# Performance work log

Measured on AMD Instinct MI355X. Metric: run time of the kernel, lower is better.

The kernel has to match this reference:

```python
import jax, jax.numpy as jnp
import numpy as np

INF = 1.0e9
B, NI, NJ = 1, 768, 768
C_NODE, C_PAIR = 512, 128
H, C_HID = 8, 32
LN_EPS = 1e-5


def _ln(x, w, b):
    m = jnp.mean(x, axis=-1, keepdims=True)
    v = jnp.mean(jnp.square(x - m), axis=-1, keepdims=True)
    return (x - m) * jax.lax.rsqrt(v + LN_EPS) * w + b


def setup_inputs() -> dict:
    key = jax.random.key(0)
    ks = jax.random.split(key, 16)
    s_node = 1.0 / np.sqrt(C_NODE)
    s_pair = 1.0 / np.sqrt(C_PAIR)
    s_hid = 1.0 / np.sqrt(H * C_HID)
    inp = {
        "node_embed_i": jax.random.normal(ks[0], (B, NI, C_NODE), jnp.float32),
        "node_embed_j": jax.random.normal(ks[1], (B, NJ, C_NODE), jnp.float32),
        "pair_embed": jax.random.normal(ks[2], (B, NI, NJ, C_PAIR), jnp.float32),
        "pair_mask": (jax.random.uniform(ks[3], (B, NI, NJ)) < 0.95).astype(jnp.float32),
        "node_mask_i": (jax.random.uniform(ks[4], (B, NI)) < 0.98).astype(jnp.float32),
        # LayerNorm params
        "ln_i_w": jnp.ones((C_NODE,), jnp.float32), "ln_i_b": jnp.zeros((C_NODE,), jnp.float32),
        "ln_j_w": jnp.ones((C_NODE,), jnp.float32), "ln_j_b": jnp.zeros((C_NODE,), jnp.float32),
        "ln_p_w": jnp.ones((C_PAIR,), jnp.float32), "ln_p_b": jnp.zeros((C_PAIR,), jnp.float32),
        # pair-bias projection and its gate: Linear(C_PAIR, H)
        "W_pb": jax.random.normal(ks[5], (C_PAIR, H), jnp.float32) * s_pair,
        "b_pb": jnp.zeros((H,), jnp.float32),
        "W_pg": jax.random.normal(ks[6], (C_PAIR, H), jnp.float32) * s_pair,
        "b_pg": jnp.zeros((H,), jnp.float32),
        # attention projections (q/k/v bias-free, OpenFold-style)
        "Wq": jax.random.normal(ks[7], (C_NODE, H * C_HID), jnp.float32) * s_node,
        "Wk": jax.random.normal(ks[8], (C_NODE, H * C_HID), jnp.float32) * s_node,
        "Wv": jax.random.normal(ks[9], (C_NODE, H * C_HID), jnp.float32) * s_node,
        # output gate and output projection
        "Wg": jax.random.normal(ks[10], (C_NODE, H * C_HID), jnp.float32) * s_node,
        "bg": jnp.zeros((H * C_HID,), jnp.float32),
        "Wo": jax.random.normal(ks[11], (H * C_HID, C_NODE), jnp.float32) * s_hid,
        "bo": jnp.zeros((C_NODE,), jnp.float32),
    }
    return inp


def reference(node_embed_i, node_embed_j, pair_embed, pair_mask, node_mask_i,
              ln_i_w, ln_i_b, ln_j_w, ln_j_b, ln_p_w, ln_p_b,
              W_pb, b_pb, W_pg, b_pg, Wq, Wk, Wv, Wg, bg, Wo, bo):
    # LayerNorms
    qx = _ln(node_embed_i, ln_i_w, ln_i_b)           # [B,NI,C_NODE]
    kx = _ln(node_embed_j, ln_j_w, ln_j_b)           # [B,NJ,C_NODE]
    p = _ln(pair_embed, ln_p_w, ln_p_b)              # [B,NI,NJ,C_PAIR]

    # additive mask bias: 0 where valid, -inf where masked; broadcast over heads
    mask_bias = (INF * (pair_mask - 1.0))[:, None, :, :]          # [B,1,NI,NJ]

    # gated pair bias -> [B,H,NI,NJ] (permute_final_dims([2,0,1]))
    pb = (p @ W_pb + b_pb) * jax.nn.sigmoid(p @ W_pg + b_pg)      # [B,NI,NJ,H]
    pair_bias = jnp.transpose(pb, (0, 3, 1, 2))

    # multi-head attention with injected biases
    q = (qx @ Wq).reshape(B, NI, H, C_HID) * (C_HID ** -0.5)
    k = (kx @ Wk).reshape(B, NJ, H, C_HID)
    v = (kx @ Wv).reshape(B, NJ, H, C_HID)
    scores = jnp.einsum('bihc,bjhc->bhij', q, k) + mask_bias + pair_bias
    a = jax.nn.softmax(scores, axis=-1)                           # [B,H,NI,NJ]
    o = jnp.einsum('bhij,bjhc->bihc', a, v)                       # [B,NI,H,C_HID]

    # sigmoid output gate, flatten heads, output projection
    g = jax.nn.sigmoid(qx @ Wg + bg).reshape(B, NI, H, C_HID)
    o = (o * g).reshape(B, NI, H * C_HID)
    mha_out = o @ Wo + bo                                         # [B,NI,C_NODE]

    # residual on the layernormed input, scaled by node mask (dropout = identity at inference)
    return qx + mha_out * node_mask_i[..., None]
```

## Files before the change

### kernel.cpp

```cpp
#include <hip/hip_runtime.h>
#include <hip/hip_bf16.h>

#define NI 768
#define NJ 768
#define CN 512
#define CP 128
#define NH 8
#define CH 32
#define HC 256
#define NSTR 6
#define SJ 128

typedef float  fx4  __attribute__((ext_vector_type(4)));
typedef float  fx2  __attribute__((ext_vector_type(2)));
typedef short  bv8  __attribute__((ext_vector_type(8)));
typedef unsigned short usx4 __attribute__((ext_vector_type(4)));

__device__ __forceinline__ short f2bf(float f) {
    __hip_bfloat16 h = __float2bfloat16(f);
    return *reinterpret_cast<short*>(&h);
}
__device__ __forceinline__ float bf2f(unsigned short u) {
    union { unsigned int u; float f; } c; c.u = ((unsigned int)u) << 16; return c.f;
}

__global__ __launch_bounds__(256) void fused_front_kernel(
    const float* __restrict__ node_i, const float* __restrict__ node_j,
    const float* __restrict__ ln_i_w, const float* __restrict__ ln_i_b,
    const float* __restrict__ ln_j_w, const float* __restrict__ ln_j_b,
    const float* __restrict__ Wq, const float* __restrict__ Wk,
    const float* __restrict__ Wv, const float* __restrict__ Wg,
    const float* __restrict__ bg,
    const float* __restrict__ lnpw, const float* __restrict__ lnpb,
    const float* __restrict__ Wpb, const float* __restrict__ bpb,
    const float* __restrict__ Wpg, const float* __restrict__ bpg,
    const float* __restrict__ pair, const float* __restrict__ pmask,
    float* __restrict__ qx, unsigned short* __restrict__ qsb,
    unsigned short* __restrict__ ksb, unsigned short* __restrict__ vtb,
    float* __restrict__ gs, unsigned short* __restrict__ biasb)
{
    const int bid = blockIdx.x;
    const int t = threadIdx.x;
    if (bid < 192) {
        __shared__ float xs[8][CN];
        __shared__ float red[4][8][2];
        const bool isj = bid >= 96;
        const int r0 = (isj ? bid - 96 : bid) * 8;
        const float* xin = isj ? node_j : node_i;
        const float* lw = isj ? ln_j_w : ln_i_w;
        const float* lb = isj ? ln_j_b : ln_i_b;
        const int wv = t >> 6;

        fx2 vrow[8]; float s8[8], q8[8];
#pragma unroll
        for (int r = 0; r < 8; ++r) {
            vrow[r] = *(const fx2*)(xin + (size_t)(r0 + r) * CN + t * 2);
            s8[r] = vrow[r][0] + vrow[r][1];
            q8[r] = vrow[r][0] * vrow[r][0] + vrow[r][1] * vrow[r][1];
        }
#pragma unroll
        for (int d = 1; d < 64; d <<= 1)
#pragma unroll
            for (int r = 0; r < 8; ++r) {
                s8[r] += __shfl_xor(s8[r], d);
                q8[r] += __shfl_xor(q8[r], d);
            }
        if ((t & 63) == 0)
#pragma unroll
            for (int r = 0; r < 8; ++r) { red[wv][r][0] = s8[r]; red[wv][r][1] = q8[r]; }
        __syncthreads();
        fx2 lwv = *(const fx2*)(lw + t * 2), lbv = *(const fx2*)(lb + t * 2);
#pragma unroll
        for (int r = 0; r < 8; ++r) {
            float s = red[0][r][0] + red[1][r][0] + red[2][r][0] + red[3][r][0];
            float q = red[0][r][1] + red[1][r][1] + red[2][r][1] + red[3][r][1];
            float mean = s * (1.f / CN);
            float var = q * (1.f / CN) - mean * mean;
            float rs = rsqrtf(var + 1e-5f);
            fx2 o;
            o[0] = (vrow[r][0] - mean) * rs * lwv[0] + lbv[0];
            o[1] = (vrow[r][1] - mean) * rs * lwv[1] + lbv[1];
            xs[r][t * 2] = o[0]; xs[r][t * 2 + 1] = o[1];
            if (!isj) *(fx2*)(qx + (size_t)(r0 + r) * CN + t * 2) = o;
        }
        __syncthreads();

        for (int m = 0; m < 2; ++m) {
            const float* W = isj ? (m ? Wv : Wk) : (m ? Wg : Wq);
            float acc[8] = {0.f,0.f,0.f,0.f,0.f,0.f,0.f,0.f};
            for (int cc = 0; cc < CN; cc += 4) {
                fx4 xv[8];
#pragma unroll
                for (int r = 0; r < 8; ++r) xv[r] = *(const fx4*)&xs[r][cc];
#pragma unroll
                for (int u = 0; u < 4; ++u) {
                    float w = W[(size_t)(cc + u) * HC + t];
#pragma unroll
                    for (int r = 0; r < 8; ++r) acc[r] = fmaf(xv[r][u], w, acc[r]);
                }
            }
            if (!isj) {
                if (m == 0) {
#pragma unroll
                    for (int r = 0; r < 8; ++r)
                        qsb[(size_t)(r0 + r) * HC + t] =
                            (unsigned short)f2bf(acc[r] * 0.17677669529663687f);
                } else {
#pragma unroll
                    for (int r = 0; r < 8; ++r)
                        gs[(size_t)(r0 + r) * HC + t] =
                            1.f / (1.f + __expf(-(acc[r] + bg[t])));
                }
            } else {
                if (m == 0) {
#pragma unroll
                    for (int r = 0; r < 8; ++r)
                        ksb[(size_t)(r0 + r) * HC + t] = (unsigned short)f2bf(acc[r]);
                } else {
                    bv8 vv;
#pragma unroll
                    for (int r = 0; r < 8; ++r) vv[r] = f2bf(acc[r]);
                    *(bv8*)&vtb[(size_t)t * NJ + r0] = vv;
                }
            }
        }
        return;
    }

    __shared__ unsigned short wcatT[16][136];
    __shared__ float redS[16][16], redC[16][16];
    __shared__ float scalS[16], scalC[16];
    __shared__ unsigned short sb[8][68];

    const int lane = t & 63;
    const int wave = t >> 6;
    const int bid2 = bid - 192;
    const int i    = bid2 / 12;
    const int jt64 = (bid2 % 12) * 64;
    const int jt   = jt64 + wave * 16;
    const int o  = lane & 15;
    const int kq = lane >> 4;

    for (int rep = 0; rep < 2; ++rep) {
        const float* prow = pair + ((size_t)i * NJ + (jt + o)) * CP + kq * 8;
        fx4 x0[4], x1[4];
#pragma unroll
        for (int s = 0; s < 4; ++s) {
            x0[s] = *(const fx4*)(prow + s * 32);
            x1[s] = *(const fx4*)(prow + s * 32 + 4);
        }

        {
            const int oo = t & 15, cg = t >> 4;
            float pS = 0.f, pC = 0.f;
#pragma unroll
            for (int e = 0; e < 8; ++e) {
                int c = cg * 8 + e;
                float w = (oo < 8) ? Wpb[c * 8 + oo] : Wpg[c * 8 + (oo - 8)];
                float wv = lnpw[c] * w;
                short b = f2bf(wv);
                wcatT[oo][c] = (unsigned short)b;
                pS += bf2f((unsigned short)b);
                pC += lnpb[c] * w;
            }
            redS[cg][oo] = pS; redC[cg][oo] = pC;
            __syncthreads();
            if (t < 16) {
                float s = 0.f, c2 = 0.f;
#pragma unroll
                for (int k = 0; k < 16; ++k) { s += redS[k][t]; c2 += redC[k][t]; }
                scalS[t] = s;
                scalC[t] = c2 + ((t < 8) ? bpb[t] : bpg[t - 8]);
            }
            __syncthreads();
        }

        bv8 bfrag[4];
#pragma unroll
        for (int s = 0; s < 4; ++s)
            bfrag[s] = *(const bv8*)&wcatT[o][s * 32 + kq * 8];
        const float spb = scalS[o];
        const float cpb = scalC[o];

        bv8 afrag[4];
#pragma unroll
        for (int s = 0; s < 4; ++s) {
#pragma unroll
            for (int u = 0; u < 4; ++u) {
                afrag[s][u]     = f2bf(x0[s][u]);
                afrag[s][u + 4] = f2bf(x1[s][u]);
            }
        }
        bv8 ones;
#pragma unroll
        for (int u = 0; u < 8; ++u) ones[u] = (short)0x3F80;

        fx4 acc  = {0.f, 0.f, 0.f, 0.f};
        fx4 accS = {0.f, 0.f, 0.f, 0.f};
        fx4 accG = {0.f, 0.f, 0.f, 0.f};
#pragma unroll
        for (int s = 0; s < 4; ++s) {
            acc  = __builtin_amdgcn_mfma_f32_16x16x32_bf16(afrag[s], bfrag[s], acc,  0, 0, 0);
            accS = __builtin_amdgcn_mfma_f32_16x16x32_bf16(afrag[s], ones,     accS, 0, 0, 0);
            accG = __builtin_amdgcn_mfma_f32_16x16x32_bf16(afrag[s], afrag[s], accG, 0, 0, 0);
        }

#pragma unroll
        for (int r = 0; r < 4; ++r) {
            const int p = kq * 4 + r;
            float sp = accS[r];
            float qp = __shfl(accG[r], kq * 20 + r);
            float mean = sp * (1.f / CP);
            float var  = qp * (1.f / CP) - mean * mean;
            float rstd = rsqrtf(var + 1e-5f);
            float pre  = rstd * (acc[r] - mean * spb) + cpb;
            float part = __shfl_xor(pre, 8);
            if (o < 8) {
                float sig = 1.f / (1.f + __expf(-part));
                int j = jt + p;
                float b = pre * sig + (pmask[(size_t)i * NJ + j] - 1.f) * 1.0e9f;
                sb[o][wave * 16 + p] = (unsigned short)f2bf(b);
            }
        }
        __syncthreads();
        if (t < 128) {
            const int oo = t >> 4, ck = t & 15;
            usx4 v;
#pragma unroll
            for (int u = 0; u < 4; ++u) v[u] = sb[oo][ck * 4 + u];
            *(usx4*)&biasb[((size_t)oo * NI + i) * NJ + jt64 + ck * 4] = v;
        }
        __syncthreads();
    }
}

__global__ __launch_bounds__(256) void attn_kernel(
    const short* __restrict__ qsb, const short* __restrict__ ksb,
    const short* __restrict__ vtb, const unsigned short* __restrict__ biasb,
    float* __restrict__ pnum, float* __restrict__ pden)
{
    __shared__ unsigned short P[32][136];
    __shared__ float sumbuf[4][32];
    const int i0 = blockIdx.x * 32;
    const int h  = blockIdx.y;
    const int jbase = blockIdx.z * SJ;
    const int pb = ((int)blockIdx.x * NH + h) * NSTR + blockIdx.z;
    const int t = threadIdx.x;
    const int w = t >> 6;
    const int lane = t & 63;
    const int rowl = lane & 15;
    const int g = lane >> 4;

    bv8 aq[2];
#pragma unroll
    for (int it = 0; it < 2; ++it)
        aq[it] = *(const bv8*)&qsb[(size_t)(i0 + it * 16 + rowl) * HC + h * CH + g * 8];

    bv8 bk[2];
#pragma unroll
    for (int jt = 0; jt < 2; ++jt) {
        const int jb = jbase + w * 32 + jt * 16;
        bk[jt] = *(const bv8*)&ksb[(size_t)(jb + rowl) * HC + h * CH + g * 8];
    }
    const unsigned short* bbase = biasb + (size_t)h * NI * NJ;
    unsigned short bl[2][2][4];
#pragma unroll
    for (int jt = 0; jt < 2; ++jt) {
        const int jb = jbase + w * 32 + jt * 16;
#pragma unroll
        for (int it = 0; it < 2; ++it)
#pragma unroll
            for (int r = 0; r < 4; ++r) {
                const int il = it * 16 + g * 4 + r;
                bl[jt][it][r] = bbase[(size_t)(i0 + il) * NJ + jb + rowl];
            }
    }

    float rs[2][4] = {{0.f,0.f,0.f,0.f},{0.f,0.f,0.f,0.f}};
#pragma unroll
    for (int jt = 0; jt < 2; ++jt) {
        const int jloc = w * 32 + jt * 16;
#pragma unroll
        for (int it = 0; it < 2; ++it) {
            fx4 acc = {0.f, 0.f, 0.f, 0.f};
            acc = __builtin_amdgcn_mfma_f32_16x16x32_bf16(aq[it], bk[jt], acc, 0, 0, 0);
#pragma unroll
            for (int r = 0; r < 4; ++r) {
                const int il = it * 16 + g * 4 + r;
                float s = acc[r] + bf2f(bl[jt][it][r]);
                float p = __expf(s);
                rs[it][r] += p;
                P[il][jloc + rowl] = (unsigned short)f2bf(p);
            }
        }
    }
#pragma unroll
    for (int it = 0; it < 2; ++it)
#pragma unroll
        for (int r = 0; r < 4; ++r) {
            float v = rs[it][r];
            v += __shfl_xor(v, 1); v += __shfl_xor(v, 2);
            v += __shfl_xor(v, 4); v += __shfl_xor(v, 8);
            rs[it][r] = v;
        }
    if (rowl == 0) {
#pragma unroll
        for (int it = 0; it < 2; ++it)
#pragma unroll
            for (int r = 0; r < 4; ++r)
                sumbuf[w][it * 16 + g * 4 + r] = rs[it][r];
    }

    const int it = w & 1, ct = w >> 1;
    bv8 vv[4];
#pragma unroll
    for (int kk = 0; kk < 4; ++kk)
        vv[kk] = *(const bv8*)&vtb[(size_t)(h * CH + ct * 16 + rowl) * NJ + jbase + kk * 32 + g * 8];

    __syncthreads();

    if (t < 32)
        pden[(size_t)pb * 32 + t] =
            sumbuf[0][t] + sumbuf[1][t] + sumbuf[2][t] + sumbuf[3][t];

    fx4 acc = {0.f, 0.f, 0.f, 0.f};
#pragma unroll
    for (int kk = 0; kk < 4; ++kk) {
        bv8 ap = *(const bv8*)&P[it * 16 + rowl][kk * 32 + g * 8];
        acc = __builtin_amdgcn_mfma_f32_16x16x32_bf16(ap, vv[kk], acc, 0, 0, 0);
    }
#pragma unroll
    for (int r = 0; r < 4; ++r) {
        const int il = it * 16 + g * 4 + r;
        pnum[(size_t)pb * 1024 + il * 32 + ct * 16 + rowl] = acc[r];
    }
}

__global__ __launch_bounds__(256) void combine_out_kernel(
    const float* __restrict__ pnum, const float* __restrict__ pden,
    const float* __restrict__ gs, const float* __restrict__ qx,
    const float* __restrict__ Wo, const float* __restrict__ bo,
    const float* __restrict__ mi, float* __restrict__ outp)
{
    __shared__ float ogl[2][HC];
    const int r0 = blockIdx.x * 2;
    const int t = threadIdx.x;
    const int h = t >> 5, c = t & 31;
#pragma unroll
    for (int r = 0; r < 2; ++r) {
        const int i = r0 + r;
        const int pb = ((i >> 5) * NH + h) * NSTR;
        const int il = i & 31;
        float n = 0.f, d = 0.f;
#pragma unroll
        for (int s = 0; s < NSTR; ++s) {
            n += pnum[(size_t)(pb + s) * 1024 + il * 32 + c];
            d += pden[(size_t)(pb + s) * 32 + il];
        }
        ogl[r][t] = n / d * gs[(size_t)i * HC + t];
    }
    __syncthreads();

    float acc[2][2] = {{0,0},{0,0}};
    for (int cc = 0; cc < HC; cc += 4) {
        fx4 xr0 = *(const fx4*)&ogl[0][cc];
        fx4 xr1 = *(const fx4*)&ogl[1][cc];
#pragma unroll
        for (int u = 0; u < 4; ++u) {
            float w0 = Wo[(size_t)(cc + u) * CN + t];
            float w1 = Wo[(size_t)(cc + u) * CN + 256 + t];
            acc[0][0] = fmaf(xr0[u], w0, acc[0][0]); acc[0][1] = fmaf(xr0[u], w1, acc[0][1]);
            acc[1][0] = fmaf(xr1[u], w0, acc[1][0]); acc[1][1] = fmaf(xr1[u], w1, acc[1][1]);
        }
    }
#pragma unroll
    for (int r = 0; r < 2; ++r) {
        float mk = mi[r0 + r];
        size_t base = (size_t)(r0 + r) * CN;
        outp[base + t]       = qx[base + t]       + (acc[r][0] + bo[t])       * mk;
        outp[base + 256 + t] = qx[base + 256 + t] + (acc[r][1] + bo[t + 256]) * mk;
    }
}

extern "C" void kernel_launch(void* const* d_in, const int* in_sizes, int n_in,
                              void* d_out, int out_size, void* d_ws, size_t ws_size,
                              hipStream_t stream)
{
    const float* node_i = (const float*)d_in[0];
    const float* node_j = (const float*)d_in[1];
    const float* pair   = (const float*)d_in[2];
    const float* pmask  = (const float*)d_in[3];
    const float* nmask  = (const float*)d_in[4];
    const float* ln_i_w = (const float*)d_in[5];
    const float* ln_i_b = (const float*)d_in[6];
    const float* ln_j_w = (const float*)d_in[7];
    const float* ln_j_b = (const float*)d_in[8];
    const float* ln_p_w = (const float*)d_in[9];
    const float* ln_p_b = (const float*)d_in[10];
    const float* W_pb   = (const float*)d_in[11];
    const float* b_pb   = (const float*)d_in[12];
    const float* W_pg   = (const float*)d_in[13];
    const float* b_pg   = (const float*)d_in[14];
    const float* Wq     = (const float*)d_in[15];
    const float* Wk     = (const float*)d_in[16];
    const float* Wv     = (const float*)d_in[17];
    const float* Wg     = (const float*)d_in[18];
    const float* bg     = (const float*)d_in[19];
    const float* Wo     = (const float*)d_in[20];
    const float* bo     = (const float*)d_in[21];
    float* outp = (float*)d_out;

    float* fw = (float*)d_ws;
    float* qx   = fw;
    float* gs   = qx + (size_t)NI * CN;
    float* pnum = gs + (size_t)NI * HC;
    float* pden = pnum + (size_t)24 * NH * NSTR * 1024;
    unsigned short* qsb = (unsigned short*)(pden + (size_t)24 * NH * NSTR * 32);
    unsigned short* ksb = qsb + (size_t)NI * HC;
    unsigned short* vtb = ksb + (size_t)NJ * HC;
    unsigned short* biasb = vtb + (size_t)HC * NJ;

    hipLaunchKernelGGL(fused_front_kernel, dim3(192 + (NI * NJ) / 64), dim3(256), 0, stream,
                       node_i, node_j, ln_i_w, ln_i_b, ln_j_w, ln_j_b,
                       Wq, Wk, Wv, Wg, bg,
                       ln_p_w, ln_p_b, W_pb, b_pb, W_pg, b_pg,
                       pair, pmask,
                       qx, qsb, ksb, vtb, gs, biasb);
    hipLaunchKernelGGL(attn_kernel, dim3(NI / 32, NH, NSTR), dim3(256), 0, stream,
                       (const short*)qsb, (const short*)ksb, (const short*)vtb,
                       biasb, pnum, pden);
    hipLaunchKernelGGL(combine_out_kernel, dim3(NI / 2), dim3(256), 0, stream,
                       pnum, pden, gs, qx, Wo, bo, nmask, outp);
}
```

Measured before the change: 124.3 us.

## Fuse all three stages into one persistent cooperative kernel with grid syncs

Adds a persistent mega-kernel that runs the node LayerNorm and projections, the pair-bias computation, the attention strips and the output combine. Each stage uses grid-stride loops and the stages are separated by cooperative grid barriers, launched with an occupancy-sized grid. It also drops the redundant two-iteration repeat of the pair-bias block, which recomputed and re-read the large pair tensor. The goal is to remove inter-kernel launch gaps and duplicated pair traffic. The trade-offs are grid-wide barrier costs and less latency hiding from the persistent scheduling. The old three-kernel path stays as a fallback.

```diff
diff --git a/kernel.cpp b/kernel.cpp
--- a/kernel.cpp
+++ b/kernel.cpp
@@ -1,5 +1,8 @@
 #include <hip/hip_runtime.h>
 #include <hip/hip_bf16.h>
+#include <hip/hip_cooperative_groups.h>
+
+namespace cg = cooperative_groups;
 
 #define NI 768
 #define NJ 768
@@ -22,6 +25,362 @@
 }
 __device__ __forceinline__ float bf2f(unsigned short u) {
     union { unsigned int u; float f; } c; c.u = ((unsigned int)u) << 16; return c.f;
+}
+
+struct NodeS { float xs[8][CN]; float red[4][8][2]; };
+struct PairS { float redS[16][16]; float redC[16][16]; unsigned short sb[8][68]; };
+struct AttnS { unsigned short P[32][136]; float sumbuf[4][32]; };
+struct CombS { float ogl[2][HC]; };
+union SmemU { NodeS n; PairS p; AttnS a; CombS c; };
+
+__global__ __launch_bounds__(256) void mega_kernel(
+    const float* __restrict__ node_i, const float* __restrict__ node_j,
+    const float* __restrict__ ln_i_w, const float* __restrict__ ln_i_b,
+    const float* __restrict__ ln_j_w, const float* __restrict__ ln_j_b,
+    const float* __restrict__ Wq, const float* __restrict__ Wk,
+    const float* __restrict__ Wv, const float* __restrict__ Wg,
+    const float* __restrict__ bg,
+    const float* __restrict__ lnpw, const float* __restrict__ lnpb,
+    const float* __restrict__ Wpb, const float* __restrict__ bpb,
+    const float* __restrict__ Wpg, const float* __restrict__ bpg,
+    const float* __restrict__ pair, const float* __restrict__ pmask,
+    const float* __restrict__ mi,
+    const float* __restrict__ Wo, const float* __restrict__ bo,
+    float* __restrict__ qx, unsigned short* __restrict__ qsb,
+    unsigned short* __restrict__ ksb, unsigned short* __restrict__ vtb,
+    float* __restrict__ gs, unsigned short* __restrict__ biasb,
+    float* __restrict__ pnum, float* __restrict__ pden,
+    float* __restrict__ outp)
+{
+    __shared__ SmemU sm;
+    __shared__ unsigned short wcatT[16][136];
+    __shared__ float scalS[16], scalC[16];
+
+    cg::grid_group gg = cg::this_grid();
+    const int bid = blockIdx.x;
+    const int gsz = gridDim.x;
+    const int t = threadIdx.x;
+    const int lane = t & 63, wave = t >> 6;
+    const int o = lane & 15, kq = lane >> 4;
+
+    {
+        const int oo = t & 15, cgi = t >> 4;
+        float pS = 0.f, pC = 0.f;
+#pragma unroll
+        for (int e = 0; e < 8; ++e) {
+            int c = cgi * 8 + e;
+            float w = (oo < 8) ? Wpb[c * 8 + oo] : Wpg[c * 8 + (oo - 8)];
+            float wv = lnpw[c] * w;
+            short b = f2bf(wv);
+            wcatT[oo][c] = (unsigned short)b;
+            pS += bf2f((unsigned short)b);
+            pC += lnpb[c] * w;
+        }
+        sm.p.redS[cgi][oo] = pS; sm.p.redC[cgi][oo] = pC;
+        __syncthreads();
+        if (t < 16) {
+            float s = 0.f, c2 = 0.f;
+#pragma unroll
+            for (int k = 0; k < 16; ++k) { s += sm.p.redS[k][t]; c2 += sm.p.redC[k][t]; }
+            scalS[t] = s;
+            scalC[t] = c2 + ((t < 8) ? bpb[t] : bpg[t - 8]);
+        }
+        __syncthreads();
+    }
+
+    for (int unit = bid; unit < 192 + (NI * NJ) / 64; unit += gsz) {
+        if (unit < 192) {
+            const bool isj = unit >= 96;
+            const int r0 = (isj ? unit - 96 : unit) * 8;
+            const float* xin = isj ? node_j : node_i;
+            const float* lw = isj ? ln_j_w : ln_i_w;
+            const float* lb = isj ? ln_j_b : ln_i_b;
+
+            fx2 vrow[8]; float s8[8], q8[8];
+#pragma unroll
+            for (int r = 0; r < 8; ++r) {
+                vrow[r] = *(const fx2*)(xin + (size_t)(r0 + r) * CN + t * 2);
+                s8[r] = vrow[r][0] + vrow[r][1];
+                q8[r] = vrow[r][0] * vrow[r][0] + vrow[r][1] * vrow[r][1];
+            }
+#pragma unroll
+            for (int d = 1; d < 64; d <<= 1)
+#pragma unroll
+                for (int r = 0; r < 8; ++r) {
+                    s8[r] += __shfl_xor(s8[r], d);
+                    q8[r] += __shfl_xor(q8[r], d);
+                }
+            if ((t & 63) == 0)
+#pragma unroll
+                for (int r = 0; r < 8; ++r) { sm.n.red[wave][r][0] = s8[r]; sm.n.red[wave][r][1] = q8[r]; }
+            __syncthreads();
+            fx2 lwv = *(const fx2*)(lw + t * 2), lbv = *(const fx2*)(lb + t * 2);
+#pragma unroll
+            for (int r = 0; r < 8; ++r) {
+                float s = sm.n.red[0][r][0] + sm.n.red[1][r][0] + sm.n.red[2][r][0] + sm.n.red[3][r][0];
+                float q = sm.n.red[0][r][1] + sm.n.red[1][r][1] + sm.n.red[2][r][1] + sm.n.red[3][r][1];
+                float mean = s * (1.f / CN);
+                float var = q * (1.f / CN) - mean * mean;
+                float rs = rsqrtf(var + 1e-5f);
+                fx2 ov;
+                ov[0] = (vrow[r][0] - mean) * rs * lwv[0] + lbv[0];
+                ov[1] = (vrow[r][1] - mean) * rs * lwv[1] + lbv[1];
+                sm.n.xs[r][t * 2] = ov[0]; sm.n.xs[r][t * 2 + 1] = ov[1];
+                if (!isj) *(fx2*)(qx + (size_t)(r0 + r) * CN + t * 2) = ov;
+            }
+            __syncthreads();
+
+            for (int m = 0; m < 2; ++m) {
+                const float* W = isj ? (m ? Wv : Wk) : (m ? Wg : Wq);
+                float acc[8] = {0.f,0.f,0.f,0.f,0.f,0.f,0.f,0.f};
+                for (int cc = 0; cc < CN; cc += 4) {
+                    fx4 xv[8];
+#pragma unroll
+                    for (int r = 0; r < 8; ++r) xv[r] = *(const fx4*)&sm.n.xs[r][cc];
+#pragma unroll
+                    for (int u = 0; u < 4; ++u) {
+                        float w = W[(size_t)(cc + u) * HC + t];
+#pragma unroll
+                        for (int r = 0; r < 8; ++r) acc[r] = fmaf(xv[r][u], w, acc[r]);
+                    }
+                }
+                if (!isj) {
+                    if (m == 0) {
+#pragma unroll
+                        for (int r = 0; r < 8; ++r)
+                            qsb[(size_t)(r0 + r) * HC + t] =
+                                (unsigned short)f2bf(acc[r] * 0.17677669529663687f);
+                    } else {
+#pragma unroll
+                        for (int r = 0; r < 8; ++r)
+                            gs[(size_t)(r0 + r) * HC + t] =
+                                1.f / (1.f + __expf(-(acc[r] + bg[t])));
+                    }
+                } else {
+                    if (m == 0) {
+#pragma unroll
+                        for (int r = 0; r < 8; ++r)
+                            ksb[(size_t)(r0 + r) * HC + t] = (unsigned short)f2bf(acc[r]);
+                    } else {
+                        bv8 vv;
+#pragma unroll
+                        for (int r = 0; r < 8; ++r) vv[r] = f2bf(acc[r]);
+                        *(bv8*)&vtb[(size_t)t * NJ + r0] = vv;
+                    }
+                }
+            }
+        } else {
+            const int bid2 = unit - 192;
+            const int i    = bid2 / 12;
+            const int jt64 = (bid2 % 12) * 64;
+            const int jt   = jt64 + wave * 16;
+
+            const float* prow = pair + ((size_t)i * NJ + (jt + o)) * CP + kq * 8;
+            fx4 x0[4], x1[4];
+#pragma unroll
+            for (int s = 0; s < 4; ++s) {
+                x0[s] = *(const fx4*)(prow + s * 32);
+                x1[s] = *(const fx4*)(prow + s * 32 + 4);
+            }
+
+            bv8 bfrag[4];
+#pragma unroll
+            for (int s = 0; s < 4; ++s)
+                bfrag[s] = *(const bv8*)&wcatT[o][s * 32 + kq * 8];
+            const float spb = scalS[o];
+            const float cpb = scalC[o];
+
+            bv8 afrag[4];
+#pragma unroll
+            for (int s = 0; s < 4; ++s) {
+#pragma unroll
+                for (int u = 0; u < 4; ++u) {
+                    afrag[s][u]     = f2bf(x0[s][u]);
+                    afrag[s][u + 4] = f2bf(x1[s][u]);
+                }
+            }
+            bv8 ones;
+#pragma unroll
+            for (int u = 0; u < 8; ++u) ones[u] = (short)0x3F80;
+
+            fx4 acc  = {0.f, 0.f, 0.f, 0.f};
+            fx4 accS = {0.f, 0.f, 0.f, 0.f};
+            fx4 accG = {0.f, 0.f, 0.f, 0.f};
+#pragma unroll
+            for (int s = 0; s < 4; ++s) {
+                acc  = __builtin_amdgcn_mfma_f32_16x16x32_bf16(afrag[s], bfrag[s], acc,  0, 0, 0);
+                accS = __builtin_amdgcn_mfma_f32_16x16x32_bf16(afrag[s], ones,     accS, 0, 0, 0);
+                accG = __builtin_amdgcn_mfma_f32_16x16x32_bf16(afrag[s], afrag[s], accG, 0, 0, 0);
+            }
+
+#pragma unroll
+            for (int r = 0; r < 4; ++r) {
+                const int p = kq * 4 + r;
+                float sp = accS[r];
+                float qp = __shfl(accG[r], kq * 20 + r);
+                float mean = sp * (1.f / CP);
+                float var  = qp * (1.f / CP) - mean * mean;
+                float rstd = rsqrtf(var + 1e-5f);
+                float pre  = rstd * (acc[r] - mean * spb) + cpb;
+                float part = __shfl_xor(pre, 8);
+                if (o < 8) {
+                    float sig = 1.f / (1.f + __expf(-part));
+                    int j = jt + p;
+                    float b = pre * sig + (pmask[(size_t)i * NJ + j] - 1.f) * 1.0e9f;
+                    sm.p.sb[o][wave * 16 + p] = (unsigned short)f2bf(b);
+                }
+            }
+            __syncthreads();
+            if (t < 128) {
+                const int oo = t >> 4, ck = t & 15;
+                usx4 v;
+#pragma unroll
+                for (int u = 0; u < 4; ++u) v[u] = sm.p.sb[oo][ck * 4 + u];
+                *(usx4*)&biasb[((size_t)oo * NI + i) * NJ + jt64 + ck * 4] = v;
+            }
+        }
+        __syncthreads();
+    }
+
+    gg.sync();
+
+    for (int unit = bid; unit < 24 * NH * NSTR; unit += gsz) {
+        const int ix = unit / (NH * NSTR);
+        const int rem = unit % (NH * NSTR);
+        const int h = rem / NSTR;
+        const int jz = rem % NSTR;
+        const int i0 = ix * 32;
+        const int jbase = jz * SJ;
+        const int pb = unit;
+        const int rowl = o, g = kq;
+
+        bv8 aq[2];
+#pragma unroll
+        for (int it = 0; it < 2; ++it)
+            aq[it] = *(const bv8*)&qsb[(size_t)(i0 + it * 16 + rowl) * HC + h * CH + g * 8];
+
+        bv8 bk[2];
+#pragma unroll
+        for (int jt = 0; jt < 2; ++jt) {
+            const int jb = jbase + wave * 32 + jt * 16;
+            bk[jt] = *(const bv8*)&ksb[(size_t)(jb + rowl) * HC + h * CH + g * 8];
+        }
+        const unsigned short* bbase = biasb + (size_t)h * NI * NJ;
+        unsigned short bl[2][2][4];
+#pragma unroll
+        for (int jt = 0; jt < 2; ++jt) {
+            const int jb = jbase + wave * 32 + jt * 16;
+#pragma unroll
+            for (int it = 0; it < 2; ++it)
+#pragma unroll
+                for (int r = 0; r < 4; ++r) {
+                    const int il = it * 16 + g * 4 + r;
+                    bl[jt][it][r] = bbase[(size_t)(i0 + il) * NJ + jb + rowl];
+                }
+        }
+
+        float rs[2][4] = {{0.f,0.f,0.f,0.f},{0.f,0.f,0.f,0.f}};
+#pragma unroll
+        for (int jt = 0; jt < 2; ++jt) {
+            const int jloc = wave * 32 + jt * 16;
+#pragma unroll
+            for (int it = 0; it < 2; ++it) {
+                fx4 acc = {0.f, 0.f, 0.f, 0.f};
+                acc = __builtin_amdgcn_mfma_f32_16x16x32_bf16(aq[it], bk[jt], acc, 0, 0, 0);
+#pragma unroll
+                for (int r = 0; r < 4; ++r) {
+                    const int il = it * 16 + g * 4 + r;
+                    float s = acc[r] + bf2f(bl[jt][it][r]);
+                    float p = __expf(s);
+                    rs[it][r] += p;
+                    sm.a.P[il][jloc + rowl] = (unsigned short)f2bf(p);
+                }
+            }
+        }
+#pragma unroll
+        for (int it = 0; it < 2; ++it)
+#pragma unroll
+            for (int r = 0; r < 4; ++r) {
+                float v = rs[it][r];
+                v += __shfl_xor(v, 1); v += __shfl_xor(v, 2);
+                v += __shfl_xor(v, 4); v += __shfl_xor(v, 8);
+                rs[it][r] = v;
+            }
+        if (rowl == 0) {
+#pragma unroll
+            for (int it = 0; it < 2; ++it)
+#pragma unroll
+                for (int r = 0; r < 4; ++r)
+                    sm.a.sumbuf[wave][it * 16 + g * 4 + r] = rs[it][r];
+        }
+
+        const int it2 = wave & 1, ct = wave >> 1;
+        bv8 vv[4];
+#pragma unroll
+        for (int kk = 0; kk < 4; ++kk)
+            vv[kk] = *(const bv8*)&vtb[(size_t)(h * CH + ct * 16 + rowl) * NJ + jbase + kk * 32 + g * 8];
+
+        __syncthreads();
+
+        if (t < 32)
+            pden[(size_t)pb * 32 + t] =
+                sm.a.sumbuf[0][t] + sm.a.sumbuf[1][t] + sm.a.sumbuf[2][t] + sm.a.sumbuf[3][t];
+
+        fx4 acc = {0.f, 0.f, 0.f, 0.f};
+#pragma unroll
+        for (int kk = 0; kk < 4; ++kk) {
+            bv8 ap = *(const bv8*)&sm.a.P[it2 * 16 + rowl][kk * 32 + g * 8];
+            acc = __builtin_amdgcn_mfma_f32_16x16x32_bf16(ap, vv[kk], acc, 0, 0, 0);
+        }
+#pragma unroll
+        for (int r = 0; r < 4; ++r) {
+            const int il = it2 * 16 + g * 4 + r;
+            pnum[(size_t)pb * 1024 + il * 32 + ct * 16 + rowl] = acc[r];
+        }
+        __syncthreads();
+    }
+
+    gg.sync();
+
+    for (int unit = bid; unit < NI / 2; unit += gsz) {
+        const int r0 = unit * 2;
+        const int h = t >> 5, c = t & 31;
+#pragma unroll
+        for (int r = 0; r < 2; ++r) {
+            const int i = r0 + r;
+            const int pb = ((i >> 5) * NH + h) * NSTR;
+            const int il = i & 31;
+            float n = 0.f, d = 0.f;
+#pragma unroll
+            for (int s = 0; s < NSTR; ++s) {
+                n += pnum[(size_t)(pb + s) * 1024 + il * 32 + c];
+                d += pden[(size_t)(pb + s) * 32 + il];
+            }
+            sm.c.ogl[r][t] = n / d * gs[(size_t)i * HC + t];
+        }
+        __syncthreads();
+
+        float acc[2][2] = {{0,0},{0,0}};
+        for (int cc = 0; cc < HC; cc += 4) {
+            fx4 xr0 = *(const fx4*)&sm.c.ogl[0][cc];
+            fx4 xr1 = *(const fx4*)&sm.c.ogl[1][cc];
+#pragma unroll
+            for (int u = 0; u < 4; ++u) {
+                float w0 = Wo[(size_t)(cc + u) * CN + t];
+                float w1 = Wo[(size_t)(cc + u) * CN + 256 + t];
+                acc[0][0] = fmaf(xr0[u], w0, acc[0][0]); acc[0][1] = fmaf(xr0[u], w1, acc[0][1]);
+                acc[1][0] = fmaf(xr1[u], w0, acc[1][0]); acc[1][1] = fmaf(xr1[u], w1, acc[1][1]);
+            }
+        }
+#pragma unroll
+        for (int r = 0; r < 2; ++r) {
+            float mk = mi[r0 + r];
+            size_t base = (size_t)(r0 + r) * CN;
+            outp[base + t]       = qx[base + t]       + (acc[r][0] + bo[t])       * mk;
+            outp[base + 256 + t] = qx[base + 256 + t] + (acc[r][1] + bo[t + 256]) * mk;
+        }
+        __syncthreads();
+    }
 }
 
 __global__ __launch_bounds__(256) void fused_front_kernel(
@@ -141,96 +500,93 @@
     const int o  = lane & 15;
     const int kq = lane >> 4;
 
-    for (int rep = 0; rep < 2; ++rep) {
-        const float* prow = pair + ((size_t)i * NJ + (jt + o)) * CP + kq * 8;
-        fx4 x0[4], x1[4];
-#pragma unroll
-        for (int s = 0; s < 4; ++s) {
-            x0[s] = *(const fx4*)(prow + s * 32);
-            x1[s] = *(const fx4*)(prow + s * 32 + 4);
-        }
-
-        {
-            const int oo = t & 15, cg = t >> 4;
-            float pS = 0.f, pC = 0.f;
-#pragma unroll
-            for (int e = 0; e < 8; ++e) {
-                int c = cg * 8 + e;
-                float w = (oo < 8) ? Wpb[c * 8 + oo] : Wpg[c * 8 + (oo - 8)];
-                float wv = lnpw[c] * w;
-                short b = f2bf(wv);
-                wcatT[oo][c] = (unsigned short)b;
-                pS += bf2f((unsigned short)b);
-                pC += lnpb[c] * w;
-            }
-            redS[cg][oo] = pS; redC[cg][oo] = pC;
-            __syncthreads();
-            if (t < 16) {
-                float s = 0.f, c2 = 0.f;
-#pragma unroll
-                for (int k = 0; k < 16; ++k) { s += redS[k][t]; c2 += redC[k][t]; }
-                scalS[t] = s;
-                scalC[t] = c2 + ((t < 8) ? bpb[t] : bpg[t - 8]);
-            }
-            __syncthreads();
-        }
-
-        bv8 bfrag[4];
-#pragma unroll
-        for (int s = 0; s < 4; ++s)
-            bfrag[s] = *(const bv8*)&wcatT[o][s * 32 + kq * 8];
-        const float spb = scalS[o];
-        const float cpb = scalC[o];
-
-        bv8 afrag[4];
-#pragma unroll
-        for (int s = 0; s < 4; ++s) {
-#pragma unroll
-            for (int u = 0; u < 4; ++u) {
-                afrag[s][u]     = f2bf(x0[s][u]);
-                afrag[s][u + 4] = f2bf(x1[s][u]);
-            }
-        }
-        bv8 ones;
-#pragma unroll
-        for (int u = 0; u < 8; ++u) ones[u] = (short)0x3F80;
-
-        fx4 acc  = {0.f, 0.f, 0.f, 0.f};
-        fx4 accS = {0.f, 0.f, 0.f, 0.f};
-        fx4 accG = {0.f, 0.f, 0.f, 0.f};
-#pragma unroll
-        for (int s = 0; s < 4; ++s) {
-            acc  = __builtin_amdgcn_mfma_f32_16x16x32_bf16(afrag[s], bfrag[s], acc,  0, 0, 0);
-            accS = __builtin_amdgcn_mfma_f32_16x16x32_bf16(afrag[s], ones,     accS, 0, 0, 0);
-            accG = __builtin_amdgcn_mfma_f32_16x16x32_bf16(afrag[s], afrag[s], accG, 0, 0, 0);
-        }
-
-#pragma unroll
-        for (int r = 0; r < 4; ++r) {
-            const int p = kq * 4 + r;
-            float sp = accS[r];
-            float qp = __shfl(accG[r], kq * 20 + r);
-            float mean = sp * (1.f / CP);
-            float var  = qp * (1.f / CP) - mean * mean;
-            float rstd = rsqrtf(var + 1e-5f);
-            float pre  = rstd * (acc[r] - mean * spb) + cpb;
-            float part = __shfl_xor(pre, 8);
-            if (o < 8) {
-                float sig = 1.f / (1.f + __expf(-part));
-                int j = jt + p;
-                float b = pre * sig + (pmask[(size_t)i * NJ + j] - 1.f) * 1.0e9f;
-                sb[o][wave * 16 + p] = (unsigned short)f2bf(b);
-            }
-        }
-        __syncthreads();
-        if (t < 128) {
-            const int oo = t >> 4, ck = t & 15;
-            usx4 v;
-#pragma unroll
-            for (int u = 0; u < 4; ++u) v[u] = sb[oo][ck * 4 + u];
-            *(usx4*)&biasb[((size_t)oo * NI + i) * NJ + jt64 + ck * 4] = v;
-        }
-        __syncthreads();
+    const float* prow = pair + ((size_t)i * NJ + (jt + o)) * CP + kq * 8;
+    fx4 x0[4], x1[4];
+#pragma unroll
+    for (int s = 0; s < 4; ++s) {
+        x0[s] = *(const fx4*)(prow + s * 32);
+        x1[s] = *(const fx4*)(prow + s * 32 + 4);
+    }
+
+    {
+        const int oo = t & 15, cgi = t >> 4;
+        float pS = 0.f, pC = 0.f;
+#pragma unroll
+        for (int e = 0; e < 8; ++e) {
+            int c = cgi * 8 + e;
+            float w = (oo < 8) ? Wpb[c * 8 + oo] : Wpg[c * 8 + (oo - 8)];
+            float wv = lnpw[c] * w;
+            short b = f2bf(wv);
+            wcatT[oo][c] = (unsigned short)b;
+            pS += bf2f((unsigned short)b);
+            pC += lnpb[c] * w;
+        }
+        redS[cgi][oo] = pS; redC[cgi][oo] = pC;
+        __syncthreads();
+        if (t < 16) {
+            float s = 0.f, c2 = 0.f;
+#pragma unroll
+            for (int k = 0; k < 16; ++k) { s += redS[k][t]; c2 += redC[k][t]; }
+            scalS[t] = s;
+            scalC[t] = c2 + ((t < 8) ? bpb[t] : bpg[t - 8]);
+        }
+        __syncthreads();
+    }
+
+    bv8 bfrag[4];
+#pragma unroll
+    for (int s = 0; s < 4; ++s)
+        bfrag[s] = *(const bv8*)&wcatT[o][s * 32 + kq * 8];
+    const float spb = scalS[o];
+    const float cpb = scalC[o];
+
+    bv8 afrag[4];
+#pragma unroll
+    for (int s = 0; s < 4; ++s) {
+#pragma unroll
+        for (int u = 0; u < 4; ++u) {
+            afrag[s][u]     = f2bf(x0[s][u]);
+            afrag[s][u + 4] = f2bf(x1[s][u]);
+        }
+    }
+    bv8 ones;
+#pragma unroll
+    for (int u = 0; u < 8; ++u) ones[u] = (short)0x3F80;
+
+    fx4 acc  = {0.f, 0.f, 0.f, 0.f};
+    fx4 accS = {0.f, 0.f, 0.f, 0.f};
+    fx4 accG = {0.f, 0.f, 0.f, 0.f};
+#pragma unroll
+    for (int s = 0; s < 4; ++s) {
+        acc  = __builtin_amdgcn_mfma_f32_16x16x32_bf16(afrag[s], bfrag[s], acc,  0, 0, 0);
+        accS = __builtin_amdgcn_mfma_f32_16x16x32_bf16(afrag[s], ones,     accS, 0, 0, 0);
+        accG = __builtin_amdgcn_mfma_f32_16x16x32_bf16(afrag[s], afrag[s], accG, 0, 0, 0);
+    }
+
+#pragma unroll
+    for (int r = 0; r < 4; ++r) {
+        const int p = kq * 4 + r;
+        float sp = accS[r];
+        float qp = __shfl(accG[r], kq * 20 + r);
+        float mean = sp * (1.f / CP);
+        float var  = qp * (1.f / CP) - mean * mean;
+        float rstd = rsqrtf(var + 1e-5f);
+        float pre  = rstd * (acc[r] - mean * spb) + cpb;
+        float part = __shfl_xor(pre, 8);
+        if (o < 8) {
+            float sig = 1.f / (1.f + __expf(-part));
+            int j = jt + p;
+            float b = pre * sig + (pmask[(size_t)i * NJ + j] - 1.f) * 1.0e9f;
+            sb[o][wave * 16 + p] = (unsigned short)f2bf(b);
+        }
+    }
+    __syncthreads();
+    if (t < 128) {
+        const int oo = t >> 4, ck = t & 15;
+        usx4 v;
+#pragma unroll
+        for (int u = 0; u < 4; ++u) v[u] = sb[oo][ck * 4 + u];
+        *(usx4*)&biasb[((size_t)oo * NI + i) * NJ + jt64 + ck * 4] = v;
     }
 }
 
@@ -420,15 +776,39 @@
     unsigned short* vtb = ksb + (size_t)NJ * HC;
     unsigned short* biasb = vtb + (size_t)HC * NJ;
 
-    hipLaunchKernelGGL(fused_front_kernel, dim3(192 + (NI * NJ) / 64), dim3(256), 0, stream,
-                       node_i, node_j, ln_i_w, ln_i_b, ln_j_w, ln_j_b,
-                       Wq, Wk, Wv, Wg, bg,
-                       ln_p_w, ln_p_b, W_pb, b_pb, W_pg, b_pg,
-                       pair, pmask,
-                       qx, qsb, ksb, vtb, gs, biasb);
-    hipLaunchKernelGGL(attn_kernel, dim3(NI / 32, NH, NSTR), dim3(256), 0, stream,
-                       (const short*)qsb, (const short*)ksb, (const short*)vtb,
-                       biasb, pnum, pden);
-    hipLaunchKernelGGL(combine_out_kernel, dim3(NI / 2), dim3(256), 0, stream,
-                       pnum, pden, gs, qx, Wo, bo, nmask, outp);
+    int nb = 0;
+    hipError_t qe = hipOccupancyMaxActiveBlocksPerMultiprocessor(&nb, mega_kernel, 256, 0);
+    bool coop_ok = (qe == hipSuccess && nb > 0);
+    if (coop_ok) {
+        int grid = nb * 256;
+        if (grid > 2048) grid = 2048;
+        void* args[] = {
+            (void*)&node_i, (void*)&node_j,
+            (void*)&ln_i_w, (void*)&ln_i_b, (void*)&ln_j_w, (void*)&ln_j_b,
+            (void*)&Wq, (void*)&Wk, (void*)&Wv, (void*)&Wg, (void*)&bg,
+            (void*)&ln_p_w, (void*)&ln_p_b, (void*)&W_pb, (void*)&b_pb,
+            (void*)&W_pg, (void*)&b_pg, (void*)&pair, (void*)&pmask,
+            (void*)&nmask, (void*)&Wo, (void*)&bo,
+            (void*)&qx, (void*)&qsb, (void*)&ksb, (void*)&vtb, (void*)&gs,
+            (void*)&biasb, (void*)&pnum, (void*)&pden, (void*)&outp
+        };
+        hipError_t le = hipLaunchCooperativeKernel((const void*)mega_kernel,
+                                                   dim3(grid), dim3(256),
+                                                   args, 0, stream);
+        if (le != hipSuccess) coop_ok = false;
+    }
+
+    if (!coop_ok) {
+        hipLaunchKernelGGL(fused_front_kernel, dim3(192 + (NI * NJ) / 64), dim3(256), 0, stream,
+                           node_i, node_j, ln_i_w, ln_i_b, ln_j_w, ln_j_b,
+                           Wq, Wk, Wv, Wg, bg,
+                           ln_p_w, ln_p_b, W_pb, b_pb, W_pg, b_pg,
+                           pair, pmask,
+                           qx, qsb, ksb, vtb, gs, biasb);
+        hipLaunchKernelGGL(attn_kernel, dim3(NI / 32, NH, NSTR), dim3(256), 0, stream,
+                           (const short*)qsb, (const short*)ksb, (const short*)vtb,
+                           biasb, pnum, pden);
+        hipLaunchKernelGGL(combine_out_kernel, dim3(NI / 2), dim3(256), 0, stream,
+                           pnum, pden, gs, qx, Wo, bo, nmask, outp);
+    }
 }
```

Measured after the change: 340.2 us. 2.74x slower.
